# Kernel tuning notes

Hardware: AMD Instinct MI355X
Metric: run time of the kernel (lower is better)

## Reference

```python
import jax, jax.numpy as jnp
import numpy as np

WIDTHS = [2, 3, 5, 8, 13, 21, 34, 55, 89, 26]  # ragged one-hot feature widths, sum = 256
NSEG = len(WIDTHS)
B, IN = 8192, 256
LAYOUT = [1024, 1024, 1024, 256]
EPS = 1e-5  # BatchNorm1d default eps
TAU = 1.0


def setup_inputs() -> dict:
    key = jax.random.key(0)
    ks = iter(jax.random.split(key, 64))
    inp = {"x": jax.random.normal(next(ks), (B, IN), jnp.float32)}
    prev = IN
    for i, fc in enumerate(LAYOUT):
        inp[f"W{i}"] = jax.random.normal(next(ks), (fc, prev), jnp.float32) / np.float32(np.sqrt(prev))
        inp[f"b{i}"] = 0.01 * jax.random.normal(next(ks), (fc,), jnp.float32)
        if i + 1 < len(LAYOUT):  # Residual blocks carry BatchNorm params (eval mode)
            inp[f"g{i}"] = 1.0 + 0.1 * jax.random.normal(next(ks), (fc,), jnp.float32)
            inp[f"be{i}"] = 0.1 * jax.random.normal(next(ks), (fc,), jnp.float32)
            inp[f"rm{i}"] = 0.1 * jax.random.normal(next(ks), (fc,), jnp.float32)
            inp[f"rv{i}"] = 0.75 + 0.5 * jax.random.uniform(next(ks), (fc,), dtype=jnp.float32)
        prev += fc
    inp["seg_ids"] = jnp.asarray(np.repeat(np.arange(NSEG), WIDTHS), jnp.int32)  # [256]
    return inp


def _residual(x, W, b, g, be, rm, rv):
    # Linear -> eval-mode BatchNorm1d -> ReLU -> concat([out, input])
    h = x @ W.T + b
    h = (h - rm) * (g * jax.lax.rsqrt(rv + EPS)) + be
    return jnp.concatenate([jax.nn.relu(h), x], axis=1)


def _segment_softmax(x, seg_ids):
    # Fused segmented softmax over ragged feature groups (replaces per-feature Python loop)
    xt = x.T / TAU                                            # [F, B]
    m = jax.ops.segment_max(xt, seg_ids, num_segments=NSEG)   # [NSEG, B]
    e = jnp.exp(xt - m[seg_ids])
    s = jax.ops.segment_sum(e, seg_ids, num_segments=NSEG)
    return (e / s[seg_ids]).T                                 # [B, F]


def reference(x, W0, b0, g0, be0, rm0, rv0, W1, b1, g1, be1, rm1, rv1,
              W2, b2, g2, be2, rm2, rv2, W3, b3, seg_ids):
    h = _residual(x, W0, b0, g0, be0, rm0, rv0)   # [B, 1280]
    h = _residual(h, W1, b1, g1, be1, rm1, rv1)   # [B, 2304]
    h = _residual(h, W2, b2, g2, be2, rm2, rv2)   # [B, 3328]
    h = h @ W3.T + b3                              # [B, 256]
    return _segment_softmax(h, seg_ids)
```

## Files before the change

### kernel.cpp

```cpp
#include <hip/hip_runtime.h>
#include <hip/hip_fp16.h>


#define LDH 3328
#define NROWS 8192

typedef _Float16 f16x8 __attribute__((ext_vector_type(8)));
typedef _Float16 f16x4 __attribute__((ext_vector_type(4)));
typedef float f32x4 __attribute__((ext_vector_type(4)));

__constant__ int c_bnd[11] = {0, 2, 5, 10, 18, 31, 52, 86, 141, 230, 256};

__device__ __forceinline__ void async_cp16(const _Float16* g, _Float16* l) {
  __builtin_amdgcn_global_load_lds(
      (__attribute__((address_space(1))) void*)g,
      (__attribute__((address_space(3))) void*)l, 16, 0, 0);
}

__device__ __forceinline__ _Float16 f2h(float f) { return (_Float16)f; }

__global__ void cvt_all_kernel(const float* __restrict__ s0,
                               const float* __restrict__ s1,
                               const float* __restrict__ s2,
                               const float* __restrict__ s3,
                               const float* __restrict__ x,
                               _Float16* __restrict__ d0,
                               _Float16* __restrict__ d1,
                               _Float16* __restrict__ d2,
                               _Float16* __restrict__ d3,
                               _Float16* __restrict__ H,
                               int n0, int n1, int n2, int n3, int n4) {
  int i = blockIdx.x * blockDim.x + threadIdx.x;
  if (i >= n4) return;
  if (i >= n3) {
    const int j = i - n3;
    const int row = j >> 6;
    const int c = (j & 63) * 4;
    const float4 v = *(const float4*)&x[(size_t)j * 4];
    f16x4 h = {f2h(v.x), f2h(v.y), f2h(v.z), f2h(v.w)};
    *(f16x4*)&H[(size_t)row * LDH + 3072 + c] = h;
    return;
  }
  const float* s;
  _Float16* d;
  if (i < n0) {
    s = s0; d = d0;
  } else if (i < n1) {
    s = s1 - (size_t)n0 * 4; d = d1 - (size_t)n0 * 4;
  } else if (i < n2) {
    s = s2 - (size_t)n1 * 4; d = d2 - (size_t)n1 * 4;
  } else {
    s = s3 - (size_t)n2 * 4; d = d3 - (size_t)n2 * 4;
  }
  const float4 v = *(const float4*)&s[(size_t)i * 4];
  f16x4 h = {f2h(v.x), f2h(v.y), f2h(v.z), f2h(v.w)};
  *(f16x4*)&d[(size_t)i * 4] = h;
}

template <int FUSE, int TN>
__launch_bounds__(256, 4) __global__
void gemm_kernel(const _Float16* __restrict__ A, int ldA, int K,
                 const _Float16* __restrict__ W,
                 const float* __restrict__ bias, const float* __restrict__ g,
                 const float* __restrict__ be, const float* __restrict__ rm,
                 const float* __restrict__ rv,
                 _Float16* __restrict__ outH, int outOff,
                 float* __restrict__ outF, int ldF) {
  constexpr int BN = TN * 32;
  __shared__ _Float16 Alds[64 * 64];
  __shared__ _Float16 Blds[BN * 64];

  const int tid = threadIdx.x;
  const int lane = tid & 63;
  const int wave = tid >> 6;
  const int wr = wave >> 1;
  const int wc = wave & 1;
  const int row0 = blockIdx.x * 64;
  const int col0 = blockIdx.y * BN;
  const int lr = lane >> 3;
  const int ls = lane & 7;
  const int lc = ls ^ lr;
  const int fr = lane & 15;
  const int q = lane >> 4;

  f32x4 acc[2][TN] = {};

  for (int k0 = 0; k0 < K; k0 += 64) {
    __syncthreads();
#pragma unroll
    for (int it = 0; it < 2; ++it) {
      const int rl = it * 32 + wave * 8;
      async_cp16(A + (size_t)(row0 + rl + lr) * ldA + k0 + lc * 8,
                 &Alds[rl * 64]);
    }
#pragma unroll
    for (int it = 0; it < TN; ++it) {
      const int rl = it * 32 + wave * 8;
      async_cp16(W + (size_t)(col0 + rl + lr) * K + k0 + lc * 8,
                 &Blds[rl * 64]);
    }
    __syncthreads();

#pragma unroll
    for (int kq = 0; kq < 2; ++kq) {
      f16x8 av[2], bv[TN];
#pragma unroll
      for (int t = 0; t < 2; ++t) {
        const int ra = wr * 32 + t * 16 + fr;
        av[t] = *(const f16x8*)&Alds[ra * 64 + (((q + 4 * kq) ^ (ra & 7)) * 8)];
      }
#pragma unroll
      for (int t = 0; t < TN; ++t) {
        const int rb = wc * (TN * 16) + t * 16 + fr;
        bv[t] = *(const f16x8*)&Blds[rb * 64 + (((q + 4 * kq) ^ (rb & 7)) * 8)];
      }
#pragma unroll
      for (int tm = 0; tm < 2; ++tm)
#pragma unroll
        for (int tn = 0; tn < TN; ++tn)
          acc[tm][tn] = __builtin_amdgcn_mfma_f32_16x16x32_f16(
              av[tm], bv[tn], acc[tm][tn], 0, 0, 0);
    }
  }

#pragma unroll
  for (int tn = 0; tn < TN; ++tn) {
    const int n = col0 + wc * (TN * 16) + tn * 16 + fr;
    if constexpr (FUSE == 1) {
      const float alpha = g[n] * rsqrtf(rv[n] + 1e-5f);
      const float beta = (bias[n] - rm[n]) * alpha + be[n];
#pragma unroll
      for (int tm = 0; tm < 2; ++tm) {
        const int rbase = row0 + wr * 32 + tm * 16 + q * 4;
#pragma unroll
        for (int r = 0; r < 4; ++r) {
          float v = acc[tm][tn][r] * alpha + beta;
          v = fmaxf(v, 0.0f);
          outH[(size_t)(rbase + r) * LDH + outOff + n] = f2h(v);
        }
      }
    } else {
      const float bb = bias[n];
#pragma unroll
      for (int tm = 0; tm < 2; ++tm) {
        const int rbase = row0 + wr * 32 + tm * 16 + q * 4;
#pragma unroll
        for (int r = 0; r < 4; ++r)
          outF[(size_t)(rbase + r) * ldF + n] = acc[tm][tn][r] + bb;
      }
    }
  }
}

__global__ void segsoftmax_kernel(float* __restrict__ out,
                                  const int* __restrict__ segids) {
  __shared__ float vals[4][256];
  __shared__ float red[4][10];
  const int w = threadIdx.x >> 6;
  const int l = threadIdx.x & 63;
  const int row = blockIdx.x * 4 + w;
  float4 v = *(float4*)&out[(size_t)row * 256 + l * 4];
  *(float4*)&vals[w][l * 4] = v;
  __syncthreads();
  if (l < 10) {
    float m = -1e30f;
    for (int j = c_bnd[l]; j < c_bnd[l + 1]; ++j) m = fmaxf(m, vals[w][j]);
    red[w][l] = m;
  }
  __syncthreads();
  const int4 s4 = *(const int4*)&segids[l * 4];
  float4 e;
  e.x = expf(v.x - red[w][s4.x]);
  e.y = expf(v.y - red[w][s4.y]);
  e.z = expf(v.z - red[w][s4.z]);
  e.w = expf(v.w - red[w][s4.w]);
  *(float4*)&vals[w][l * 4] = e;
  __syncthreads();
  if (l < 10) {
    float s = 0.0f;
    for (int j = c_bnd[l]; j < c_bnd[l + 1]; ++j) s += vals[w][j];
    red[w][l] = s;
  }
  __syncthreads();
  float4 o;
  o.x = e.x / red[w][s4.x];
  o.y = e.y / red[w][s4.y];
  o.z = e.z / red[w][s4.z];
  o.w = e.w / red[w][s4.w];
  *(float4*)&out[(size_t)row * 256 + l * 4] = o;
}

extern "C" void kernel_launch(void* const* d_in, const int* in_sizes, int n_in,
                              void* d_out, int out_size, void* d_ws,
                              size_t ws_size, hipStream_t stream) {
  const float* x = (const float*)d_in[0];
  const float* W0 = (const float*)d_in[1];
  const float* b0 = (const float*)d_in[2];
  const float* g0 = (const float*)d_in[3];
  const float* be0 = (const float*)d_in[4];
  const float* rm0 = (const float*)d_in[5];
  const float* rv0 = (const float*)d_in[6];
  const float* W1 = (const float*)d_in[7];
  const float* b1 = (const float*)d_in[8];
  const float* g1 = (const float*)d_in[9];
  const float* be1 = (const float*)d_in[10];
  const float* rm1 = (const float*)d_in[11];
  const float* rv1 = (const float*)d_in[12];
  const float* W2 = (const float*)d_in[13];
  const float* b2 = (const float*)d_in[14];
  const float* g2 = (const float*)d_in[15];
  const float* be2 = (const float*)d_in[16];
  const float* rm2 = (const float*)d_in[17];
  const float* rv2 = (const float*)d_in[18];
  const float* W3 = (const float*)d_in[19];
  const float* b3 = (const float*)d_in[20];
  const int* seg = (const int*)d_in[21];
  float* out = (float*)d_out;

  _Float16* H = (_Float16*)d_ws;
  size_t off = (size_t)NROWS * LDH;
  _Float16* Wh0 = H + off; off += 1024 * 256;
  _Float16* Wh1 = H + off; off += 1024 * 1280;
  _Float16* Wh2 = H + off; off += 1024 * 2304;
  _Float16* Wh3 = H + off;

  const int n0 = 65536, n1 = n0 + 327680, n2 = n1 + 589824, n3 = n2 + 212992;
  const int n4 = n3 + 524288;
  cvt_all_kernel<<<(n4 + 255) / 256, 256, 0, stream>>>(
      W0, W1, W2, W3, x, Wh0, Wh1, Wh2, Wh3, H, n0, n1, n2, n3, n4);

  dim3 blk(256);
  gemm_kernel<1, 4><<<dim3(128, 8), blk, 0, stream>>>(
      H + 3072, LDH, 256, Wh0, b0, g0, be0, rm0, rv0, H, 2048, nullptr, 0);
  gemm_kernel<1, 4><<<dim3(128, 8), blk, 0, stream>>>(
      H + 2048, LDH, 1280, Wh1, b1, g1, be1, rm1, rv1, H, 1024, nullptr, 0);
  gemm_kernel<1, 4><<<dim3(128, 8), blk, 0, stream>>>(
      H + 1024, LDH, 2304, Wh2, b2, g2, be2, rm2, rv2, H, 0, nullptr, 0);
  gemm_kernel<0, 2><<<dim3(128, 4), blk, 0, stream>>>(
      H, LDH, 3328, Wh3, b3, nullptr, nullptr, nullptr, nullptr, nullptr, 0,
      out, 256);
  segsoftmax_kernel<<<2048, 256, 0, stream>>>(out, seg);
}
```

Baseline: 256.7 us.

## Fuse all layers into a persistent megakernel with grid barriers and split-K final GEMM

Replaces the six separate launches (convert, four GEMMs, softmax) with one persistent kernel of 512 blocks that runs each stage in turn, separated by atomic-counter grid barriers. GEMM tiles grow to 128x128 with a 4x4 MFMA accumulator per wave. The last GEMM is split four ways along K and accumulated with float atomicAdd into an output pre-filled with the bias. The intent is to remove launch gaps and tail effects and to raise per-tile data reuse. In exchange it relies on all 512 blocks being co-resident for the barriers to avoid deadlock, uses fewer waves per CU, and makes the final sum order nondeterministic through the atomics.

Result: slower. 542.0 us (+111.1%).

```diff
diff --git a/kernel.cpp b/kernel.cpp
--- a/kernel.cpp
+++ b/kernel.cpp
@@ -4,6 +4,7 @@
 
 #define LDH 3328
 #define NROWS 8192
+#define NBLK 512
 
 typedef _Float16 f16x8 __attribute__((ext_vector_type(8)));
 typedef _Float16 f16x4 __attribute__((ext_vector_type(4)));
@@ -19,83 +20,61 @@
 
 __device__ __forceinline__ _Float16 f2h(float f) { return (_Float16)f; }
 
-__global__ void cvt_all_kernel(const float* __restrict__ s0,
-                               const float* __restrict__ s1,
-                               const float* __restrict__ s2,
-                               const float* __restrict__ s3,
-                               const float* __restrict__ x,
-                               _Float16* __restrict__ d0,
-                               _Float16* __restrict__ d1,
-                               _Float16* __restrict__ d2,
-                               _Float16* __restrict__ d3,
-                               _Float16* __restrict__ H,
-                               int n0, int n1, int n2, int n3, int n4) {
-  int i = blockIdx.x * blockDim.x + threadIdx.x;
-  if (i >= n4) return;
-  if (i >= n3) {
-    const int j = i - n3;
-    const int row = j >> 6;
-    const int c = (j & 63) * 4;
-    const float4 v = *(const float4*)&x[(size_t)j * 4];
-    f16x4 h = {f2h(v.x), f2h(v.y), f2h(v.z), f2h(v.w)};
-    *(f16x4*)&H[(size_t)row * LDH + 3072 + c] = h;
-    return;
-  }
-  const float* s;
-  _Float16* d;
-  if (i < n0) {
-    s = s0; d = d0;
-  } else if (i < n1) {
-    s = s1 - (size_t)n0 * 4; d = d1 - (size_t)n0 * 4;
-  } else if (i < n2) {
-    s = s2 - (size_t)n1 * 4; d = d2 - (size_t)n1 * 4;
-  } else {
-    s = s3 - (size_t)n2 * 4; d = d3 - (size_t)n2 * 4;
-  }
-  const float4 v = *(const float4*)&s[(size_t)i * 4];
-  f16x4 h = {f2h(v.x), f2h(v.y), f2h(v.z), f2h(v.w)};
-  *(f16x4*)&d[(size_t)i * 4] = h;
-}
-
-template <int FUSE, int TN>
-__launch_bounds__(256, 4) __global__
-void gemm_kernel(const _Float16* __restrict__ A, int ldA, int K,
-                 const _Float16* __restrict__ W,
-                 const float* __restrict__ bias, const float* __restrict__ g,
-                 const float* __restrict__ be, const float* __restrict__ rm,
-                 const float* __restrict__ rv,
-                 _Float16* __restrict__ outH, int outOff,
-                 float* __restrict__ outF, int ldF) {
-  constexpr int BN = TN * 32;
-  __shared__ _Float16 Alds[64 * 64];
-  __shared__ _Float16 Blds[BN * 64];
+__device__ __forceinline__ void gridbar(unsigned* c, unsigned target) {
+  __syncthreads();
+  if (threadIdx.x == 0) {
+    __threadfence();
+    atomicAdd(c, 1u);
+    while (__hip_atomic_load(c, __ATOMIC_RELAXED, __HIP_MEMORY_SCOPE_AGENT) <
+           target)
+      __builtin_amdgcn_s_sleep(8);
+    __threadfence();
+  }
+  __syncthreads();
+}
+
+__global__ void zero_kernel(unsigned* c) { *c = 0u; }
+
+template <int FUSE, int NCB>
+__device__ __forceinline__ void gemm_phase(
+    unsigned char* smem, const _Float16* __restrict__ A, int ldA, int K,
+    int kSpan, const _Float16* __restrict__ W, const float* __restrict__ bias,
+    const float* __restrict__ g, const float* __restrict__ be,
+    const float* __restrict__ rm, const float* __restrict__ rv,
+    _Float16* __restrict__ outH, int outOff, float* __restrict__ outF,
+    int ldF) {
+  _Float16* Alds = (_Float16*)smem;
+  _Float16* Blds = (_Float16*)(smem + 16384);
 
   const int tid = threadIdx.x;
   const int lane = tid & 63;
   const int wave = tid >> 6;
   const int wr = wave >> 1;
   const int wc = wave & 1;
-  const int row0 = blockIdx.x * 64;
-  const int col0 = blockIdx.y * BN;
+  const int t = blockIdx.x;
+  const int bx = t & 63;
+  const int rest = t >> 6;
+  const int cb = rest % NCB;
+  const int ks = rest / NCB;
+  const int row0 = bx * 128;
+  const int col0 = cb * 128;
+  const int k0b = ks * kSpan;
+  const int k0e = k0b + kSpan;
   const int lr = lane >> 3;
   const int ls = lane & 7;
   const int lc = ls ^ lr;
   const int fr = lane & 15;
   const int q = lane >> 4;
 
-  f32x4 acc[2][TN] = {};
-
-  for (int k0 = 0; k0 < K; k0 += 64) {
+  f32x4 acc[4][4] = {};
+
+  for (int k0 = k0b; k0 < k0e; k0 += 64) {
     __syncthreads();
 #pragma unroll
-    for (int it = 0; it < 2; ++it) {
+    for (int it = 0; it < 4; ++it) {
       const int rl = it * 32 + wave * 8;
       async_cp16(A + (size_t)(row0 + rl + lr) * ldA + k0 + lc * 8,
                  &Alds[rl * 64]);
-    }
-#pragma unroll
-    for (int it = 0; it < TN; ++it) {
-      const int rl = it * 32 + wave * 8;
       async_cp16(W + (size_t)(col0 + rl + lr) * K + k0 + lc * 8,
                  &Blds[rl * 64]);
     }
@@ -103,35 +82,34 @@
 
 #pragma unroll
     for (int kq = 0; kq < 2; ++kq) {
-      f16x8 av[2], bv[TN];
-#pragma unroll
-      for (int t = 0; t < 2; ++t) {
-        const int ra = wr * 32 + t * 16 + fr;
-        av[t] = *(const f16x8*)&Alds[ra * 64 + (((q + 4 * kq) ^ (ra & 7)) * 8)];
-      }
-#pragma unroll
-      for (int t = 0; t < TN; ++t) {
-        const int rb = wc * (TN * 16) + t * 16 + fr;
-        bv[t] = *(const f16x8*)&Blds[rb * 64 + (((q + 4 * kq) ^ (rb & 7)) * 8)];
-      }
-#pragma unroll
-      for (int tm = 0; tm < 2; ++tm)
-#pragma unroll
-        for (int tn = 0; tn < TN; ++tn)
+      f16x8 av[4], bv[4];
+#pragma unroll
+      for (int tt = 0; tt < 4; ++tt) {
+        const int ra = wr * 64 + tt * 16 + fr;
+        av[tt] =
+            *(const f16x8*)&Alds[ra * 64 + (((q + 4 * kq) ^ (ra & 7)) * 8)];
+        const int rb = wc * 64 + tt * 16 + fr;
+        bv[tt] =
+            *(const f16x8*)&Blds[rb * 64 + (((q + 4 * kq) ^ (rb & 7)) * 8)];
+      }
+#pragma unroll
+      for (int tm = 0; tm < 4; ++tm)
+#pragma unroll
+        for (int tn = 0; tn < 4; ++tn)
           acc[tm][tn] = __builtin_amdgcn_mfma_f32_16x16x32_f16(
               av[tm], bv[tn], acc[tm][tn], 0, 0, 0);
     }
   }
 
 #pragma unroll
-  for (int tn = 0; tn < TN; ++tn) {
-    const int n = col0 + wc * (TN * 16) + tn * 16 + fr;
+  for (int tn = 0; tn < 4; ++tn) {
+    const int n = col0 + wc * 64 + tn * 16 + fr;
     if constexpr (FUSE == 1) {
       const float alpha = g[n] * rsqrtf(rv[n] + 1e-5f);
       const float beta = (bias[n] - rm[n]) * alpha + be[n];
 #pragma unroll
-      for (int tm = 0; tm < 2; ++tm) {
-        const int rbase = row0 + wr * 32 + tm * 16 + q * 4;
+      for (int tm = 0; tm < 4; ++tm) {
+        const int rbase = row0 + wr * 64 + tm * 16 + q * 4;
 #pragma unroll
         for (int r = 0; r < 4; ++r) {
           float v = acc[tm][tn][r] * alpha + beta;
@@ -140,54 +118,127 @@
         }
       }
     } else {
-      const float bb = bias[n];
-#pragma unroll
-      for (int tm = 0; tm < 2; ++tm) {
-        const int rbase = row0 + wr * 32 + tm * 16 + q * 4;
+#pragma unroll
+      for (int tm = 0; tm < 4; ++tm) {
+        const int rbase = row0 + wr * 64 + tm * 16 + q * 4;
 #pragma unroll
         for (int r = 0; r < 4; ++r)
-          outF[(size_t)(rbase + r) * ldF + n] = acc[tm][tn][r] + bb;
-      }
-    }
-  }
-}
-
-__global__ void segsoftmax_kernel(float* __restrict__ out,
-                                  const int* __restrict__ segids) {
-  __shared__ float vals[4][256];
-  __shared__ float red[4][10];
-  const int w = threadIdx.x >> 6;
-  const int l = threadIdx.x & 63;
-  const int row = blockIdx.x * 4 + w;
-  float4 v = *(float4*)&out[(size_t)row * 256 + l * 4];
-  *(float4*)&vals[w][l * 4] = v;
-  __syncthreads();
-  if (l < 10) {
-    float m = -1e30f;
-    for (int j = c_bnd[l]; j < c_bnd[l + 1]; ++j) m = fmaxf(m, vals[w][j]);
-    red[w][l] = m;
-  }
-  __syncthreads();
-  const int4 s4 = *(const int4*)&segids[l * 4];
-  float4 e;
-  e.x = expf(v.x - red[w][s4.x]);
-  e.y = expf(v.y - red[w][s4.y]);
-  e.z = expf(v.z - red[w][s4.z]);
-  e.w = expf(v.w - red[w][s4.w]);
-  *(float4*)&vals[w][l * 4] = e;
-  __syncthreads();
-  if (l < 10) {
-    float s = 0.0f;
-    for (int j = c_bnd[l]; j < c_bnd[l + 1]; ++j) s += vals[w][j];
-    red[w][l] = s;
-  }
-  __syncthreads();
-  float4 o;
-  o.x = e.x / red[w][s4.x];
-  o.y = e.y / red[w][s4.y];
-  o.z = e.z / red[w][s4.z];
-  o.w = e.w / red[w][s4.w];
-  *(float4*)&out[(size_t)row * 256 + l * 4] = o;
+          atomicAdd(&outF[(size_t)(rbase + r) * ldF + n], acc[tm][tn][r]);
+      }
+    }
+  }
+}
+
+__launch_bounds__(256, 2) __global__ void mega_kernel(
+    const float* __restrict__ x, const float* __restrict__ W0,
+    const float* __restrict__ b0, const float* __restrict__ g0,
+    const float* __restrict__ be0, const float* __restrict__ rm0,
+    const float* __restrict__ rv0, const float* __restrict__ W1,
+    const float* __restrict__ b1, const float* __restrict__ g1,
+    const float* __restrict__ be1, const float* __restrict__ rm1,
+    const float* __restrict__ rv1, const float* __restrict__ W2,
+    const float* __restrict__ b2, const float* __restrict__ g2,
+    const float* __restrict__ be2, const float* __restrict__ rm2,
+    const float* __restrict__ rv2, const float* __restrict__ W3,
+    const float* __restrict__ b3, const int* __restrict__ seg,
+    float* __restrict__ out, _Float16* __restrict__ H,
+    _Float16* __restrict__ Wh0, _Float16* __restrict__ Wh1,
+    _Float16* __restrict__ Wh2, _Float16* __restrict__ Wh3, unsigned* cnt) {
+  __shared__ __align__(16) unsigned char smem[32768];
+  const int tid = threadIdx.x;
+
+  {
+    const int n0 = 65536;
+    const int n1 = n0 + 327680;
+    const int n2 = n1 + 589824;
+    const int n3 = n2 + 212992;
+    const int n4 = n3 + 524288;
+    const int n5 = n4 + 524288;
+    for (int i = blockIdx.x * 256 + tid; i < n5; i += NBLK * 256) {
+      if (i < n3) {
+        const float* s;
+        _Float16* d;
+        if (i < n0) {
+          s = W0; d = Wh0;
+        } else if (i < n1) {
+          s = W1 - (size_t)n0 * 4; d = Wh1 - (size_t)n0 * 4;
+        } else if (i < n2) {
+          s = W2 - (size_t)n1 * 4; d = Wh2 - (size_t)n1 * 4;
+        } else {
+          s = W3 - (size_t)n2 * 4; d = Wh3 - (size_t)n2 * 4;
+        }
+        const float4 v = *(const float4*)&s[(size_t)i * 4];
+        f16x4 h = {f2h(v.x), f2h(v.y), f2h(v.z), f2h(v.w)};
+        *(f16x4*)&d[(size_t)i * 4] = h;
+      } else if (i < n4) {
+        const int j = i - n3;
+        const int row = j >> 6;
+        const int c = (j & 63) * 4;
+        const float4 v = *(const float4*)&x[(size_t)j * 4];
+        f16x4 h = {f2h(v.x), f2h(v.y), f2h(v.z), f2h(v.w)};
+        *(f16x4*)&H[(size_t)row * LDH + 3072 + c] = h;
+      } else {
+        const int j = i - n4;
+        const int c = (j & 63) * 4;
+        *(float4*)&out[(size_t)j * 4] = *(const float4*)&b3[c];
+      }
+    }
+  }
+  gridbar(cnt, 1 * NBLK);
+
+  gemm_phase<1, 8>(smem, H + 3072, LDH, 256, 256, Wh0, b0, g0, be0, rm0, rv0,
+                   H, 2048, nullptr, 0);
+  gridbar(cnt, 2 * NBLK);
+  gemm_phase<1, 8>(smem, H + 2048, LDH, 1280, 1280, Wh1, b1, g1, be1, rm1,
+                   rv1, H, 1024, nullptr, 0);
+  gridbar(cnt, 3 * NBLK);
+  gemm_phase<1, 8>(smem, H + 1024, LDH, 2304, 2304, Wh2, b2, g2, be2, rm2,
+                   rv2, H, 0, nullptr, 0);
+  gridbar(cnt, 4 * NBLK);
+  gemm_phase<0, 2>(smem, H, LDH, 3328, 832, Wh3, nullptr, nullptr, nullptr,
+                   nullptr, nullptr, nullptr, 0, out, 256);
+  gridbar(cnt, 5 * NBLK);
+
+  {
+    float(*vals)[256] = (float(*)[256])smem;
+    float(*red)[16] = (float(*)[16])(smem + 4096 + 128);
+    const int w = tid >> 6;
+    const int l = tid & 63;
+    const int4 s4 = *(const int4*)&seg[l * 4];
+#pragma unroll 1
+    for (int batch = 0; batch < 4; ++batch) {
+      const int row = blockIdx.x * 16 + batch * 4 + w;
+      __syncthreads();
+      float4 v = *(float4*)&out[(size_t)row * 256 + l * 4];
+      *(float4*)&vals[w][l * 4] = v;
+      __syncthreads();
+      if (l < 10) {
+        float m = -1e30f;
+        for (int j = c_bnd[l]; j < c_bnd[l + 1]; ++j) m = fmaxf(m, vals[w][j]);
+        red[w][l] = m;
+      }
+      __syncthreads();
+      float4 e;
+      e.x = expf(v.x - red[w][s4.x]);
+      e.y = expf(v.y - red[w][s4.y]);
+      e.z = expf(v.z - red[w][s4.z]);
+      e.w = expf(v.w - red[w][s4.w]);
+      *(float4*)&vals[w][l * 4] = e;
+      __syncthreads();
+      if (l < 10) {
+        float s = 0.0f;
+        for (int j = c_bnd[l]; j < c_bnd[l + 1]; ++j) s += vals[w][j];
+        red[w][l] = s;
+      }
+      __syncthreads();
+      float4 o;
+      o.x = e.x / red[w][s4.x];
+      o.y = e.y / red[w][s4.y];
+      o.z = e.z / red[w][s4.z];
+      o.w = e.w / red[w][s4.w];
+      *(float4*)&out[(size_t)row * 256 + l * 4] = o;
+    }
+  }
 }
 
 extern "C" void kernel_launch(void* const* d_in, const int* in_sizes, int n_in,
@@ -222,22 +273,11 @@
   _Float16* Wh0 = H + off; off += 1024 * 256;
   _Float16* Wh1 = H + off; off += 1024 * 1280;
   _Float16* Wh2 = H + off; off += 1024 * 2304;
-  _Float16* Wh3 = H + off;
-
-  const int n0 = 65536, n1 = n0 + 327680, n2 = n1 + 589824, n3 = n2 + 212992;
-  const int n4 = n3 + 524288;
-  cvt_all_kernel<<<(n4 + 255) / 256, 256, 0, stream>>>(
-      W0, W1, W2, W3, x, Wh0, Wh1, Wh2, Wh3, H, n0, n1, n2, n3, n4);
-
-  dim3 blk(256);
-  gemm_kernel<1, 4><<<dim3(128, 8), blk, 0, stream>>>(
-      H + 3072, LDH, 256, Wh0, b0, g0, be0, rm0, rv0, H, 2048, nullptr, 0);
-  gemm_kernel<1, 4><<<dim3(128, 8), blk, 0, stream>>>(
-      H + 2048, LDH, 1280, Wh1, b1, g1, be1, rm1, rv1, H, 1024, nullptr, 0);
-  gemm_kernel<1, 4><<<dim3(128, 8), blk, 0, stream>>>(
-      H + 1024, LDH, 2304, Wh2, b2, g2, be2, rm2, rv2, H, 0, nullptr, 0);
-  gemm_kernel<0, 2><<<dim3(128, 4), blk, 0, stream>>>(
-      H, LDH, 3328, Wh3, b3, nullptr, nullptr, nullptr, nullptr, nullptr, 0,
-      out, 256);
-  segsoftmax_kernel<<<2048, 256, 0, stream>>>(out, seg);
-}
+  _Float16* Wh3 = H + off; off += 256 * 3328;
+  unsigned* cnt = (unsigned*)(H + off);
+
+  zero_kernel<<<1, 1, 0, stream>>>(cnt);
+  mega_kernel<<<NBLK, 256, 0, stream>>>(
+      x, W0, b0, g0, be0, rm0, rv0, W1, b1, g1, be1, rm1, rv1, W2, b2, g2,
+      be2, rm2, rv2, W3, b3, seg, out, H, Wh0, Wh1, Wh2, Wh3, cnt);
+}
```

## Use 128x128 GEMM tiles, split-K final GEMM with atomics and fused softmax

Applied to the files above, without the earlier changes.

Enlarges the GEMM block tile from 64x128 to 128x128 so each wave computes a 64x64 sub-tile, raising MFMA work per LDS load. The final GEMM is split four ways along K, and partial sums are accumulated with float atomics into an output pre-filled with the bias in the prep kernel. A per-row-block counter lets the last-finishing block run the segmented softmax in place, which removes the separate softmax launch. The trade-offs are fewer blocks per BN layer (512 instead of 1024), atomic traffic on the output, and a serialized softmax tail inside a single block.

Measured after the change: 638.3 us. 2.49x slower.

```diff
diff --git a/kernel.cpp b/kernel.cpp
--- a/kernel.cpp
+++ b/kernel.cpp
@@ -19,19 +19,28 @@
 
 __device__ __forceinline__ _Float16 f2h(float f) { return (_Float16)f; }
 
-__global__ void cvt_all_kernel(const float* __restrict__ s0,
-                               const float* __restrict__ s1,
-                               const float* __restrict__ s2,
-                               const float* __restrict__ s3,
-                               const float* __restrict__ x,
-                               _Float16* __restrict__ d0,
-                               _Float16* __restrict__ d1,
-                               _Float16* __restrict__ d2,
-                               _Float16* __restrict__ d3,
-                               _Float16* __restrict__ H,
-                               int n0, int n1, int n2, int n3, int n4) {
+__global__ void prep_kernel(const float* __restrict__ s0,
+                            const float* __restrict__ s1,
+                            const float* __restrict__ s2,
+                            const float* __restrict__ s3,
+                            const float* __restrict__ x,
+                            const float* __restrict__ b3,
+                            _Float16* __restrict__ d0,
+                            _Float16* __restrict__ d1,
+                            _Float16* __restrict__ d2,
+                            _Float16* __restrict__ d3,
+                            _Float16* __restrict__ H, float* __restrict__ out,
+                            unsigned* __restrict__ cnt, int n0, int n1,
+                            int n2, int n3, int n4, int n5) {
   int i = blockIdx.x * blockDim.x + threadIdx.x;
-  if (i >= n4) return;
+  if (blockIdx.x == 0 && threadIdx.x < 64) cnt[threadIdx.x] = 0u;
+  if (i >= n5) return;
+  if (i >= n4) {
+    const int j = i - n4;
+    const int c = (j & 63) * 4;
+    *(float4*)&out[(size_t)j * 4] = *(const float4*)&b3[c];
+    return;
+  }
   if (i >= n3) {
     const int j = i - n3;
     const int row = j >> 6;
@@ -57,45 +66,39 @@
   *(f16x4*)&d[(size_t)i * 4] = h;
 }
 
-template <int FUSE, int TN>
 __launch_bounds__(256, 4) __global__
-void gemm_kernel(const _Float16* __restrict__ A, int ldA, int K,
-                 const _Float16* __restrict__ W,
-                 const float* __restrict__ bias, const float* __restrict__ g,
-                 const float* __restrict__ be, const float* __restrict__ rm,
-                 const float* __restrict__ rv,
-                 _Float16* __restrict__ outH, int outOff,
-                 float* __restrict__ outF, int ldF) {
-  constexpr int BN = TN * 32;
-  __shared__ _Float16 Alds[64 * 64];
-  __shared__ _Float16 Blds[BN * 64];
+void gemm_bn_kernel(const _Float16* __restrict__ A, int K,
+                    const _Float16* __restrict__ W,
+                    const float* __restrict__ bias,
+                    const float* __restrict__ g, const float* __restrict__ be,
+                    const float* __restrict__ rm,
+                    const float* __restrict__ rv, _Float16* __restrict__ outH,
+                    int outOff) {
+  __shared__ _Float16 Alds[128 * 64];
+  __shared__ _Float16 Blds[128 * 64];
 
   const int tid = threadIdx.x;
   const int lane = tid & 63;
   const int wave = tid >> 6;
   const int wr = wave >> 1;
   const int wc = wave & 1;
-  const int row0 = blockIdx.x * 64;
-  const int col0 = blockIdx.y * BN;
+  const int row0 = blockIdx.x * 128;
+  const int col0 = blockIdx.y * 128;
   const int lr = lane >> 3;
   const int ls = lane & 7;
   const int lc = ls ^ lr;
   const int fr = lane & 15;
   const int q = lane >> 4;
 
-  f32x4 acc[2][TN] = {};
+  f32x4 acc[4][4] = {};
 
   for (int k0 = 0; k0 < K; k0 += 64) {
     __syncthreads();
 #pragma unroll
-    for (int it = 0; it < 2; ++it) {
+    for (int it = 0; it < 4; ++it) {
       const int rl = it * 32 + wave * 8;
-      async_cp16(A + (size_t)(row0 + rl + lr) * ldA + k0 + lc * 8,
+      async_cp16(A + (size_t)(row0 + rl + lr) * LDH + k0 + lc * 8,
                  &Alds[rl * 64]);
-    }
-#pragma unroll
-    for (int it = 0; it < TN; ++it) {
-      const int rl = it * 32 + wave * 8;
       async_cp16(W + (size_t)(col0 + rl + lr) * K + k0 + lc * 8,
                  &Blds[rl * 64]);
     }
@@ -103,91 +106,159 @@
 
 #pragma unroll
     for (int kq = 0; kq < 2; ++kq) {
-      f16x8 av[2], bv[TN];
-#pragma unroll
-      for (int t = 0; t < 2; ++t) {
-        const int ra = wr * 32 + t * 16 + fr;
+      f16x8 av[4], bv[4];
+#pragma unroll
+      for (int t = 0; t < 4; ++t) {
+        const int ra = wr * 64 + t * 16 + fr;
         av[t] = *(const f16x8*)&Alds[ra * 64 + (((q + 4 * kq) ^ (ra & 7)) * 8)];
-      }
-#pragma unroll
-      for (int t = 0; t < TN; ++t) {
-        const int rb = wc * (TN * 16) + t * 16 + fr;
+        const int rb = wc * 64 + t * 16 + fr;
         bv[t] = *(const f16x8*)&Blds[rb * 64 + (((q + 4 * kq) ^ (rb & 7)) * 8)];
       }
 #pragma unroll
-      for (int tm = 0; tm < 2; ++tm)
-#pragma unroll
-        for (int tn = 0; tn < TN; ++tn)
+      for (int tm = 0; tm < 4; ++tm)
+#pragma unroll
+        for (int tn = 0; tn < 4; ++tn)
           acc[tm][tn] = __builtin_amdgcn_mfma_f32_16x16x32_f16(
               av[tm], bv[tn], acc[tm][tn], 0, 0, 0);
     }
   }
 
 #pragma unroll
-  for (int tn = 0; tn < TN; ++tn) {
-    const int n = col0 + wc * (TN * 16) + tn * 16 + fr;
-    if constexpr (FUSE == 1) {
-      const float alpha = g[n] * rsqrtf(rv[n] + 1e-5f);
-      const float beta = (bias[n] - rm[n]) * alpha + be[n];
-#pragma unroll
-      for (int tm = 0; tm < 2; ++tm) {
-        const int rbase = row0 + wr * 32 + tm * 16 + q * 4;
-#pragma unroll
-        for (int r = 0; r < 4; ++r) {
-          float v = acc[tm][tn][r] * alpha + beta;
-          v = fmaxf(v, 0.0f);
-          outH[(size_t)(rbase + r) * LDH + outOff + n] = f2h(v);
-        }
+  for (int tn = 0; tn < 4; ++tn) {
+    const int n = col0 + wc * 64 + tn * 16 + fr;
+    const float alpha = g[n] * rsqrtf(rv[n] + 1e-5f);
+    const float beta = (bias[n] - rm[n]) * alpha + be[n];
+#pragma unroll
+    for (int tm = 0; tm < 4; ++tm) {
+      const int rbase = row0 + wr * 64 + tm * 16 + q * 4;
+#pragma unroll
+      for (int r = 0; r < 4; ++r) {
+        float v = acc[tm][tn][r] * alpha + beta;
+        v = fmaxf(v, 0.0f);
+        outH[(size_t)(rbase + r) * LDH + outOff + n] = f2h(v);
       }
-    } else {
-      const float bb = bias[n];
-#pragma unroll
-      for (int tm = 0; tm < 2; ++tm) {
-        const int rbase = row0 + wr * 32 + tm * 16 + q * 4;
-#pragma unroll
-        for (int r = 0; r < 4; ++r)
-          outF[(size_t)(rbase + r) * ldF + n] = acc[tm][tn][r] + bb;
+    }
+  }
+}
+
+__launch_bounds__(256, 4) __global__
+void gemm_out_kernel(const _Float16* __restrict__ A,
+                     const _Float16* __restrict__ W, float* __restrict__ out,
+                     const int* __restrict__ seg, unsigned* __restrict__ cnt) {
+  __shared__ __align__(16) unsigned char smem[32768];
+  _Float16* Alds = (_Float16*)smem;
+  _Float16* Blds = (_Float16*)(smem + 16384);
+
+  const int tid = threadIdx.x;
+  const int lane = tid & 63;
+  const int wave = tid >> 6;
+  const int wr = wave >> 1;
+  const int wc = wave & 1;
+  const int bx = blockIdx.x;
+  const int row0 = bx * 128;
+  const int cb = blockIdx.y & 1;
+  const int ks = blockIdx.y >> 1;
+  const int col0 = cb * 128;
+  const int k0b = ks * 832;
+  const int k0e = k0b + 832;
+  const int lr = lane >> 3;
+  const int ls = lane & 7;
+  const int lc = ls ^ lr;
+  const int fr = lane & 15;
+  const int q = lane >> 4;
+  const int K = 3328;
+
+  f32x4 acc[4][4] = {};
+
+  for (int k0 = k0b; k0 < k0e; k0 += 64) {
+    __syncthreads();
+#pragma unroll
+    for (int it = 0; it < 4; ++it) {
+      const int rl = it * 32 + wave * 8;
+      async_cp16(A + (size_t)(row0 + rl + lr) * LDH + k0 + lc * 8,
+                 &Alds[rl * 64]);
+      async_cp16(W + (size_t)(col0 + rl + lr) * K + k0 + lc * 8,
+                 &Blds[rl * 64]);
+    }
+    __syncthreads();
+
+#pragma unroll
+    for (int kq = 0; kq < 2; ++kq) {
+      f16x8 av[4], bv[4];
+#pragma unroll
+      for (int t = 0; t < 4; ++t) {
+        const int ra = wr * 64 + t * 16 + fr;
+        av[t] = *(const f16x8*)&Alds[ra * 64 + (((q + 4 * kq) ^ (ra & 7)) * 8)];
+        const int rb = wc * 64 + t * 16 + fr;
+        bv[t] = *(const f16x8*)&Blds[rb * 64 + (((q + 4 * kq) ^ (rb & 7)) * 8)];
       }
-    }
-  }
-}
-
-__global__ void segsoftmax_kernel(float* __restrict__ out,
-                                  const int* __restrict__ segids) {
-  __shared__ float vals[4][256];
-  __shared__ float red[4][10];
-  const int w = threadIdx.x >> 6;
-  const int l = threadIdx.x & 63;
-  const int row = blockIdx.x * 4 + w;
-  float4 v = *(float4*)&out[(size_t)row * 256 + l * 4];
-  *(float4*)&vals[w][l * 4] = v;
+#pragma unroll
+      for (int tm = 0; tm < 4; ++tm)
+#pragma unroll
+        for (int tn = 0; tn < 4; ++tn)
+          acc[tm][tn] = __builtin_amdgcn_mfma_f32_16x16x32_f16(
+              av[tm], bv[tn], acc[tm][tn], 0, 0, 0);
+    }
+  }
+
+#pragma unroll
+  for (int tn = 0; tn < 4; ++tn) {
+    const int n = col0 + wc * 64 + tn * 16 + fr;
+#pragma unroll
+    for (int tm = 0; tm < 4; ++tm) {
+      const int rbase = row0 + wr * 64 + tm * 16 + q * 4;
+#pragma unroll
+      for (int r = 0; r < 4; ++r)
+        atomicAdd(&out[(size_t)(rbase + r) * 256 + n], acc[tm][tn][r]);
+    }
+  }
+
+  __threadfence();
   __syncthreads();
-  if (l < 10) {
-    float m = -1e30f;
-    for (int j = c_bnd[l]; j < c_bnd[l + 1]; ++j) m = fmaxf(m, vals[w][j]);
-    red[w][l] = m;
-  }
+  __shared__ unsigned last;
+  if (tid == 0) last = (atomicAdd(&cnt[bx], 1u) == 7u) ? 1u : 0u;
   __syncthreads();
-  const int4 s4 = *(const int4*)&segids[l * 4];
-  float4 e;
-  e.x = expf(v.x - red[w][s4.x]);
-  e.y = expf(v.y - red[w][s4.y]);
-  e.z = expf(v.z - red[w][s4.z]);
-  e.w = expf(v.w - red[w][s4.w]);
-  *(float4*)&vals[w][l * 4] = e;
-  __syncthreads();
-  if (l < 10) {
-    float s = 0.0f;
-    for (int j = c_bnd[l]; j < c_bnd[l + 1]; ++j) s += vals[w][j];
-    red[w][l] = s;
-  }
-  __syncthreads();
-  float4 o;
-  o.x = e.x / red[w][s4.x];
-  o.y = e.y / red[w][s4.y];
-  o.z = e.z / red[w][s4.z];
-  o.w = e.w / red[w][s4.w];
-  *(float4*)&out[(size_t)row * 256 + l * 4] = o;
+  if (!last) return;
+  __threadfence();
+
+  float(*vals)[256] = (float(*)[256])smem;
+  float(*red)[16] = (float(*)[16])(smem + 8192);
+  const int w = wave;
+  const int l = lane;
+  const int4 s4 = *(const int4*)&seg[l * 4];
+#pragma unroll 1
+  for (int batch = 0; batch < 32; ++batch) {
+    const int row = row0 + batch * 4 + w;
+    __syncthreads();
+    float4 v = *(float4*)&out[(size_t)row * 256 + l * 4];
+    *(float4*)&vals[w][l * 4] = v;
+    __syncthreads();
+    if (l < 10) {
+      float m = -1e30f;
+      for (int j = c_bnd[l]; j < c_bnd[l + 1]; ++j) m = fmaxf(m, vals[w][j]);
+      red[w][l] = m;
+    }
+    __syncthreads();
+    float4 e;
+    e.x = expf(v.x - red[w][s4.x]);
+    e.y = expf(v.y - red[w][s4.y]);
+    e.z = expf(v.z - red[w][s4.z]);
+    e.w = expf(v.w - red[w][s4.w]);
+    *(float4*)&vals[w][l * 4] = e;
+    __syncthreads();
+    if (l < 10) {
+      float s = 0.0f;
+      for (int j = c_bnd[l]; j < c_bnd[l + 1]; ++j) s += vals[w][j];
+      red[w][l] = s;
+    }
+    __syncthreads();
+    float4 o;
+    o.x = e.x / red[w][s4.x];
+    o.y = e.y / red[w][s4.y];
+    o.z = e.z / red[w][s4.z];
+    o.w = e.w / red[w][s4.w];
+    *(float4*)&out[(size_t)row * 256 + l * 4] = o;
+  }
 }
 
 extern "C" void kernel_launch(void* const* d_in, const int* in_sizes, int n_in,
@@ -222,22 +293,21 @@
   _Float16* Wh0 = H + off; off += 1024 * 256;
   _Float16* Wh1 = H + off; off += 1024 * 1280;
   _Float16* Wh2 = H + off; off += 1024 * 2304;
-  _Float16* Wh3 = H + off;
+  _Float16* Wh3 = H + off; off += 256 * 3328;
+  unsigned* cnt = (unsigned*)(H + off);
 
   const int n0 = 65536, n1 = n0 + 327680, n2 = n1 + 589824, n3 = n2 + 212992;
-  const int n4 = n3 + 524288;
-  cvt_all_kernel<<<(n4 + 255) / 256, 256, 0, stream>>>(
-      W0, W1, W2, W3, x, Wh0, Wh1, Wh2, Wh3, H, n0, n1, n2, n3, n4);
+  const int n4 = n3 + 524288, n5 = n4 + 524288;
+  prep_kernel<<<(n5 + 255) / 256, 256, 0, stream>>>(
+      W0, W1, W2, W3, x, b3, Wh0, Wh1, Wh2, Wh3, H, out, cnt, n0, n1, n2, n3,
+      n4, n5);
 
   dim3 blk(256);
-  gemm_kernel<1, 4><<<dim3(128, 8), blk, 0, stream>>>(
-      H + 3072, LDH, 256, Wh0, b0, g0, be0, rm0, rv0, H, 2048, nullptr, 0);
-  gemm_kernel<1, 4><<<dim3(128, 8), blk, 0, stream>>>(
-      H + 2048, LDH, 1280, Wh1, b1, g1, be1, rm1, rv1, H, 1024, nullptr, 0);
-  gemm_kernel<1, 4><<<dim3(128, 8), blk, 0, stream>>>(
-      H + 1024, LDH, 2304, Wh2, b2, g2, be2, rm2, rv2, H, 0, nullptr, 0);
-  gemm_kernel<0, 2><<<dim3(128, 4), blk, 0, stream>>>(
-      H, LDH, 3328, Wh3, b3, nullptr, nullptr, nullptr, nullptr, nullptr, 0,
-      out, 256);
-  segsoftmax_kernel<<<2048, 256, 0, stream>>>(out, seg);
-}
+  gemm_bn_kernel<<<dim3(64, 8), blk, 0, stream>>>(
+      H + 3072, 256, Wh0, b0, g0, be0, rm0, rv0, H, 2048);
+  gemm_bn_kernel<<<dim3(64, 8), blk, 0, stream>>>(
+      H + 2048, 1280, Wh1, b1, g1, be1, rm1, rv1, H, 1024);
+  gemm_bn_kernel<<<dim3(64, 8), blk, 0, stream>>>(
+      H + 1024, 2304, Wh2, b2, g2, be2, rm2, rv2, H, 0);
+  gemm_out_kernel<<<dim3(64, 8), blk, 0, stream>>>(H, Wh3, out, seg, cnt);
+}
```
